# Kernel tuning notes

Hardware: AMD Instinct MI355X
Metric: run time of the kernel (lower is better)

Reference implementation:

```python
import jax, jax.numpy as jnp
import numpy as np

S, D, H = 2048, 1024, 16
DH = D // H
EPS = 1e-5


def setup_inputs() -> dict:
    key = jax.random.key(0)
    ks = jax.random.split(key, 6)
    scale = 0.02
    return {
        "inputs": jax.random.normal(ks[0], (S, D), dtype=jnp.float32),
        "ln_w": jnp.ones((D,), dtype=jnp.float32),
        "ln_b": jnp.zeros((D,), dtype=jnp.float32),
        "Wq": jax.random.normal(ks[1], (D, D), dtype=jnp.float32) * scale,
        "Wk": jax.random.normal(ks[2], (D, D), dtype=jnp.float32) * scale,
        "Wv": jax.random.normal(ks[3], (D, D), dtype=jnp.float32) * scale,
        "Wo": jax.random.normal(ks[4], (D, D), dtype=jnp.float32) * scale,
    }


def reference(inputs, ln_w, ln_b, Wq, Wk, Wv, Wo):
    # Pre-LayerNorm (per token), matching eqx.nn.LayerNorm (eps=1e-5)
    mu = jnp.mean(inputs, axis=-1, keepdims=True)
    var = jnp.var(inputs, axis=-1, keepdims=True)
    x = (inputs - mu) / jnp.sqrt(var + EPS) * ln_w + ln_b  # [S, D]

    # QKV projections (eqx Linear: y = W @ x, no bias) -> [S, H, DH]
    q = (x @ Wq.T).reshape(S, H, DH)
    k = (x @ Wk.T).reshape(S, H, DH)
    v = (x @ Wv.T).reshape(S, H, DH)

    # Scaled dot-product attention; softmax forced to full precision
    scores = jnp.einsum("shd,thd->hst", q, k) / jnp.sqrt(jnp.asarray(DH, x.dtype))
    attn = jax.nn.softmax(scores.astype(jnp.float32), axis=-1).astype(x.dtype)
    # (dropout is identity in inference mode)
    ctx = jnp.einsum("hst,thd->shd", attn, v).reshape(S, D)

    out = ctx @ Wo.T  # output projection
    # outer dropout is identity in inference mode; residual add
    return out + inputs
```

## Files before the change

### kernel.cpp

```cpp
#include <hip/hip_runtime.h>
#include <cstdint>
#include <cstddef>

typedef unsigned short u16;
typedef unsigned int u32;
typedef __attribute__((ext_vector_type(8))) short bf16x8;
typedef __attribute__((ext_vector_type(4))) short bf16x4;
typedef __attribute__((ext_vector_type(4))) float f32x4;
typedef __attribute__((ext_vector_type(4))) unsigned short u16x4;

#if __has_builtin(__builtin_amdgcn_mfma_f32_16x16x16bf16_1k)
#define MFMA16(a, b, c) __builtin_amdgcn_mfma_f32_16x16x16bf16_1k(a, b, c, 0, 0, 0)
#else
static __device__ __forceinline__ f32x4 mfma16_asm(bf16x4 a, bf16x4 b, f32x4 c) {
  asm volatile("v_mfma_f32_16x16x16_bf16 %0, %1, %2, %0\n\ts_nop 4"
               : "+v"(c) : "v"(a), "v"(b));
  return c;
}
#define MFMA16(a, b, c) mfma16_asm(a, b, c)
#endif

#if __has_builtin(__builtin_amdgcn_exp2f)
#define EXP2(x) __builtin_amdgcn_exp2f(x)
#else
#define EXP2(x) exp2f(x)
#endif

__device__ __forceinline__ u16 f2b(float f) {
  union { float f; unsigned u; } un; un.f = f;
  unsigned u = un.u;
  return (u16)((u + 0x7fffu + ((u >> 16) & 1u)) >> 16);
}

__device__ __forceinline__ u32 pkbf(float a, float b) {
  union { float f; u32 u; } ua, ub; ua.f = a; ub.f = b;
  return ((ua.u + 0x8000u) >> 16) | (((ub.u + 0x8000u) >> 16) << 16);
}

__device__ __forceinline__ void gload_lds16(const u16* g, u16* l) {
  __builtin_amdgcn_global_load_lds(
      (const __attribute__((address_space(1))) void*)g,
      (__attribute__((address_space(3))) void*)l, 16, 0, 0);
}

__device__ __forceinline__ void gemm128x64(
    const u16* __restrict__ A, const u16* __restrict__ B,
    u16* smA, u16* smB, int bm, int bn,
    float* outf, u16* outb, const float* __restrict__ resid, int ostride)
{
  const int tid = threadIdx.x;
  const int wave = tid >> 6, lane = tid & 63;
  const int quad = lane >> 4, l16 = lane & 15;
  const int wm = wave >> 1, wn = wave & 1;

  f32x4 acc[4][2];
  const f32x4 zero4 = {0.f, 0.f, 0.f, 0.f};
#pragma unroll
  for (int i = 0; i < 4; i++)
#pragma unroll
    for (int j = 0; j < 2; j++) acc[i][j] = zero4;

  const u16* Ab = A + (size_t)(bm * 128) * 1024;
  const u16* Bb = B + (size_t)(bn * 64) * 1024;

#define PSTAGE(buf, k0)                                                          \
  {                                                                              \
    _Pragma("unroll")                                                            \
    for (int ks = 0; ks < 2; ks++) {                                             \
      _Pragma("unroll")                                                          \
      for (int r = 0; r < 2; r++) {                                              \
        const int c = r * 256 + wave * 64 + lane;                                \
        gload_lds16(Ab + (size_t)(c >> 2) * 1024 + (k0) + ks * 32 + (c & 3) * 8, \
                    smA + (buf) * 8192 + ks * 4096 + (size_t)(r * 256 + wave * 64) * 8); \
      }                                                                          \
      const int c2 = wave * 64 + lane;                                           \
      gload_lds16(Bb + (size_t)(c2 >> 2) * 1024 + (k0) + ks * 32 + (c2 & 3) * 8, \
                  smB + (buf) * 4096 + ks * 2048 + (size_t)(wave * 64) * 8);     \
    }                                                                            \
  }

  PSTAGE(0, 0);
  __syncthreads();
  for (int t = 0; t < 16; t++) {
    const int cur = t & 1;
    if (t < 15) PSTAGE(cur ^ 1, (t + 1) * 64);
    const u16* sa = smA + cur * 8192;
    const u16* sb = smB + cur * 4096;
#pragma unroll
    for (int ks = 0; ks < 2; ks++) {
      bf16x8 afr[4], bfr[2];
#pragma unroll
      for (int tt = 0; tt < 4; tt++)
        afr[tt] = *(const bf16x8*)(sa + ks * 4096 + (wm * 64 + tt * 16 + l16) * 32 + quad * 8);
#pragma unroll
      for (int tt = 0; tt < 2; tt++)
        bfr[tt] = *(const bf16x8*)(sb + ks * 2048 + (wn * 32 + tt * 16 + l16) * 32 + quad * 8);
#pragma unroll
      for (int mt = 0; mt < 4; mt++)
#pragma unroll
        for (int nt = 0; nt < 2; nt++)
          acc[mt][nt] = __builtin_amdgcn_mfma_f32_16x16x32_bf16(afr[mt], bfr[nt], acc[mt][nt], 0, 0, 0);
    }
    __syncthreads();
  }
#undef PSTAGE

#pragma unroll
  for (int mt = 0; mt < 4; mt++)
#pragma unroll
    for (int nt = 0; nt < 2; nt++)
#pragma unroll
      for (int r = 0; r < 4; r++) {
        const int row = bm * 128 + wm * 64 + mt * 16 + quad * 4 + r;
        const int col = bn * 64 + wn * 32 + nt * 16 + l16;
        if (outb) outb[(size_t)row * ostride + col] = f2b(acc[mt][nt][r]);
        else outf[(size_t)row * ostride + col] =
                 acc[mt][nt][r] + resid[(size_t)row * ostride + col];
      }
}

__global__ __launch_bounds__(256, 3) void proj_k(
    const u16* __restrict__ xb, const u16* __restrict__ Wb,
    u16* __restrict__ qkbuf, u16* __restrict__ vTb)
{
  __shared__ u16 smA[2 * 128 * 64];
  __shared__ u16 smB[2 * 64 * 64];
  int b = blockIdx.x;
  const u16 *A, *B; u16* o; int bm, bn;
  if (b < 512) {
    const int c = b & 7, i = b >> 3;
    bm = ((c >> 2) << 3) | (i & 7);
    bn = ((c & 3) << 3) | (i >> 3);
    A = xb; B = Wb; o = qkbuf;
  } else {
    b -= 512;
    const int c = b & 7, i = b >> 3;
    bm = i & 7;
    bn = (c << 2) | (i >> 3);
    A = Wb + (size_t)2 * (1 << 20); B = xb; o = vTb;
  }
  gemm128x64(A, B, smA, smB, bm, bn, nullptr, o, nullptr, 2048);
}

__global__ __launch_bounds__(256, 3) void out_k(
    const u16* __restrict__ ctxb, const u16* __restrict__ Wob,
    float* __restrict__ out, const float* __restrict__ x)
{
  __shared__ u16 smA[2 * 128 * 64];
  __shared__ u16 smB[2 * 64 * 64];
  const int b = blockIdx.x;
  const int c = b & 7, i = b >> 3;
  const int bm = ((c >> 2) << 3) | (i & 7);
  const int bn = ((c & 3) << 2) | (i >> 3);
  gemm128x64(ctxb, Wob, smA, smB, bm, bn, out, nullptr, x, 1024);
}

__global__ __launch_bounds__(256) void pre_k(
    const float* __restrict__ x, const float* __restrict__ lnw, const float* __restrict__ lnb,
    const float* __restrict__ w0, const float* __restrict__ w1,
    const float* __restrict__ w2, const float* __restrict__ w3,
    u16* __restrict__ xb, u16* __restrict__ Wb)
{
  const int b = blockIdx.x;
  const int tid = threadIdx.x;
  if (b < 2048) {
    const int s = b;
    const float4 v = ((const float4*)(x + (size_t)s * 1024))[tid];
    float sum = v.x + v.y + v.z + v.w;
    float sq  = v.x * v.x + v.y * v.y + v.z * v.z + v.w * v.w;
#pragma unroll
    for (int off = 32; off >= 1; off >>= 1) {
      sum += __shfl_down(sum, off);
      sq  += __shfl_down(sq, off);
    }
    __shared__ float sS[4], sQ[4];
    const int wave = tid >> 6, lane = tid & 63;
    if (lane == 0) { sS[wave] = sum; sQ[wave] = sq; }
    __syncthreads();
    const float ts = sS[0] + sS[1] + sS[2] + sS[3];
    const float tq = sQ[0] + sQ[1] + sQ[2] + sQ[3];
    const float mu = ts * (1.0f / 1024.0f);
    const float var = tq * (1.0f / 1024.0f) - mu * mu;
    const float rstd = rsqrtf(var + 1e-5f);
    const float4 wv = ((const float4*)lnw)[tid];
    const float4 bv = ((const float4*)lnb)[tid];
    u16x4 o;
    o[0] = f2b((v.x - mu) * rstd * wv.x + bv.x);
    o[1] = f2b((v.y - mu) * rstd * wv.y + bv.y);
    o[2] = f2b((v.z - mu) * rstd * wv.z + bv.z);
    o[3] = f2b((v.w - mu) * rstd * wv.w + bv.w);
    *(u16x4*)(xb + (size_t)s * 1024 + tid * 4) = o;
  } else {
    const unsigned i = (unsigned)(b - 2048) * 1024u + tid * 4u;
    const unsigned NW = 1u << 20;
    const float* src; unsigned loc; float sc;
    if (i < NW)            { src = w0; loc = i;           sc = 0.18033688f; }
    else if (i < 2u * NW)  { src = w1; loc = i - NW;      sc = 1.0f; }
    else if (i < 3u * NW)  { src = w2; loc = i - 2u * NW; sc = 1.0f; }
    else                   { src = w3; loc = i - 3u * NW; sc = 1.0f; }
    const float4 v = *(const float4*)(src + loc);
    u16x4 r;
    r[0] = f2b(v.x * sc); r[1] = f2b(v.y * sc); r[2] = f2b(v.z * sc); r[3] = f2b(v.w * sc);
    *(u16x4*)(Wb + i) = r;
  }
}

__global__ __launch_bounds__(256, 2) void attn_k(
    const u16* __restrict__ qkbuf,
    const u16* __restrict__ vT,
    u16* __restrict__ ctx)
{
  const int bid = blockIdx.x;
  const int work = (bid & 7) * 64 + (bid >> 3);
  const int h = work >> 5;
  const int q0 = (work & 31) * 64;
  __shared__ __align__(16) unsigned char arena[65536];
  u16* kvbuf = (u16*)arena;
  const int tid = threadIdx.x;
  const int wave = tid >> 6, lane = tid & 63;
  const int quad = lane >> 4, l16 = lane & 15;
  const int a7 = l16 & 7;
  const u16* kg = qkbuf + 1024;

  bf16x8 qf[4][2];
#pragma unroll
  for (int s = 0; s < 4; s++)
#pragma unroll
    for (int ks = 0; ks < 2; ks++)
      qf[s][ks] = *(const bf16x8*)(qkbuf + (size_t)(q0 + s * 16 + l16) * 2048 + h * 64 + ks * 32 + quad * 8);

  const f32x4 zero4 = {0.f, 0.f, 0.f, 0.f};
  f32x4 Oacc[4][4];
#pragma unroll
  for (int s = 0; s < 4; s++)
#pragma unroll
    for (int dt = 0; dt < 4; dt++) Oacc[s][dt] = zero4;
  float lacc[4] = {0.f, 0.f, 0.f, 0.f};

#define STAGE(T, bf)                                                                     \
  {                                                                                      \
    _Pragma("unroll")                                                                    \
    for (int i = 0; i < 4; i++) {                                                        \
      const int idx = (wave * 4 + i) * 64 + lane;                                        \
      const int kt = idx >> 3, kc = (idx & 7) ^ (kt & 7);                                \
      gload_lds16(kg + (size_t)((T) * 128 + kt) * 2048 + h * 64 + kc * 8,                \
                  kvbuf + (bf) * 16384 + (size_t)(wave * 4 + i) * 512);                  \
      const int vd = idx >> 4, vc = (idx & 15) ^ (vd & 7);                               \
      gload_lds16(vT + (size_t)(h * 64 + vd) * 2048 + (T) * 128 + vc * 8,                \
                  kvbuf + (bf) * 16384 + 8192 + (size_t)(wave * 4 + i) * 512);           \
    }                                                                                    \
  }

  STAGE(0, 0);
  __syncthreads();

  for (int T = 0; T < 16; T++) {
    const int bf = T & 1;
    if (T + 1 < 16) STAGE(T + 1, 1 - bf);
    const u16* kb = kvbuf + bf * 16384;
    const u16* vb = kb + 8192;

    f32x4 st[2][4];
#pragma unroll
    for (int ntl = 0; ntl < 2; ntl++) {
      const int nt = wave * 2 + ntl;
      const u16* kr = kb + (nt * 16 + l16) * 64;
      const bf16x8 ka0 = *(const bf16x8*)(kr + (quad ^ a7) * 8);
      const bf16x8 ka1 = *(const bf16x8*)(kr + ((4 + quad) ^ a7) * 8);
#pragma unroll
      for (int s = 0; s < 4; s++) {
        f32x4 t0 = __builtin_amdgcn_mfma_f32_16x16x32_bf16(ka0, qf[s][0], zero4, 0, 0, 0);
        st[ntl][s] = __builtin_amdgcn_mfma_f32_16x16x32_bf16(ka1, qf[s][1], t0, 0, 0, 0);
      }
    }

    bf16x4 pk[2][4];
#pragma unroll
    for (int ntl = 0; ntl < 2; ntl++)
#pragma unroll
      for (int s = 0; s < 4; s++) {
        const float p0 = EXP2(st[ntl][s][0]);
        const float p1 = EXP2(st[ntl][s][1]);
        const float p2 = EXP2(st[ntl][s][2]);
        const float p3 = EXP2(st[ntl][s][3]);
        lacc[s] += (p0 + p1) + (p2 + p3);
        union { u32 u[2]; bf16x4 v; } pp;
        pp.u[0] = pkbf(p0, p1);
        pp.u[1] = pkbf(p2, p3);
        pk[ntl][s] = pp.v;
      }

#pragma unroll
    for (int ntl = 0; ntl < 2; ntl++)
#pragma unroll
      for (int dt = 0; dt < 4; dt++) {
        const bf16x4 bv = *(const bf16x4*)(vb + (dt * 16 + l16) * 128 +
            (((wave * 4 + ntl * 2 + (quad >> 1)) ^ a7) * 8 + (quad & 1) * 4));
#pragma unroll
        for (int s = 0; s < 4; s++)
          Oacc[s][dt] = MFMA16(pk[ntl][s], bv, Oacc[s][dt]);
      }
    __syncthreads();
  }
#undef STAGE

  float* rl = (float*)arena;
#pragma unroll
  for (int s = 0; s < 4; s++) {
    float l = lacc[s];
    l += __shfl_xor(l, 16);
    l += __shfl_xor(l, 32);
    if (quad == 0) rl[wave * 64 + s * 16 + l16] = l;
  }
  __syncthreads();
  const int m = tid >> 2, dg = (tid & 3) * 16;
  const float inv = 1.0f / (rl[m] + rl[64 + m] + rl[128 + m] + rl[192 + m]);
  __syncthreads();

  float* ro = (float*)arena;
#pragma unroll
  for (int s = 0; s < 4; s++)
#pragma unroll
    for (int dt = 0; dt < 4; dt++)
#pragma unroll
      for (int r = 0; r < 4; r++) {
        const int mr = s * 16 + quad * 4 + r;
        const int dc = (dt * 16 + l16) ^ ((mr & 7) << 1);
        ro[wave * 4096 + mr * 64 + dc] = Oacc[s][dt][r];
      }
  __syncthreads();
  u16* dst = ctx + (size_t)(q0 + m) * 1024 + h * 64 + dg;
  const int msw = (m & 7) << 1;
#pragma unroll
  for (int g = 0; g < 4; g++) {
    u16x4 o;
#pragma unroll
    for (int j = 0; j < 4; j++) {
      const int dc = (dg + g * 4 + j) ^ msw;
      const int base = m * 64 + dc;
      const float v = ro[base] + ro[4096 + base] + ro[8192 + base] + ro[12288 + base];
      o[j] = f2b(v * inv);
    }
    *(u16x4*)(dst + g * 4) = o;
  }
}

extern "C" void kernel_launch(void* const* d_in, const int* in_sizes, int n_in,
                              void* d_out, int out_size, void* d_ws, size_t ws_size,
                              hipStream_t stream)
{
  const float* x   = (const float*)d_in[0];
  const float* lnw = (const float*)d_in[1];
  const float* lnb = (const float*)d_in[2];
  const float* Wq  = (const float*)d_in[3];
  const float* Wk  = (const float*)d_in[4];
  const float* Wv  = (const float*)d_in[5];
  const float* Wo  = (const float*)d_in[6];

  u16* ws    = (u16*)d_ws;
  u16* xb    = ws;
  u16* Wb    = xb + (size_t)2048 * 1024;
  u16* qkbuf = Wb + (size_t)4 * 1024 * 1024;
  u16* vTb   = qkbuf + (size_t)2048 * 2048;
  u16* ctxb  = vTb + (size_t)1024 * 2048;

  pre_k<<<6144, 256, 0, stream>>>(x, lnw, lnb, Wq, Wk, Wv, Wo, xb, Wb);
  proj_k<<<768, 256, 0, stream>>>(xb, Wb, qkbuf, vTb);
  attn_k<<<512, 256, 0, stream>>>(qkbuf, vTb, ctxb);
  out_k<<<256, 256, 0, stream>>>(ctxb, Wb + (size_t)3 * (1 << 20), (float*)d_out, x);
}
```

Measured before the change: 153.8 us.

## Enlarge GEMM tiles to 128x128 with XOR-swizzled LDS layout

The projection and output GEMMs now use 128x128 block tiles instead of 128x64, so each wave computes 64x64 and each loaded fragment is reused more. The LDS staging layout changes from two 32-wide k-slabs to a 64-wide row with an XOR swizzle, which is meant to avoid bank conflicts on fragment reads. The grids are halved (384 and 128 blocks) and occupancy drops to two blocks per SM. On a GPU with this many CUs, 128 blocks for out_k may leave many CUs idle.

Measured after the change: 150.8 us. -2.0%, faster.

```diff
diff --git a/kernel.cpp b/kernel.cpp
--- a/kernel.cpp
+++ b/kernel.cpp
@@ -43,7 +43,7 @@
       (__attribute__((address_space(3))) void*)l, 16, 0, 0);
 }
 
-__device__ __forceinline__ void gemm128x64(
+__device__ __forceinline__ void gemm128x128(
     const u16* __restrict__ A, const u16* __restrict__ B,
     u16* smA, u16* smB, int bm, int bn,
     float* outf, u16* outb, const float* __restrict__ resid, int ostride)
@@ -53,29 +53,27 @@
   const int quad = lane >> 4, l16 = lane & 15;
   const int wm = wave >> 1, wn = wave & 1;
 
-  f32x4 acc[4][2];
+  f32x4 acc[4][4];
   const f32x4 zero4 = {0.f, 0.f, 0.f, 0.f};
 #pragma unroll
   for (int i = 0; i < 4; i++)
 #pragma unroll
-    for (int j = 0; j < 2; j++) acc[i][j] = zero4;
+    for (int j = 0; j < 4; j++) acc[i][j] = zero4;
 
   const u16* Ab = A + (size_t)(bm * 128) * 1024;
-  const u16* Bb = B + (size_t)(bn * 64) * 1024;
+  const u16* Bb = B + (size_t)(bn * 128) * 1024;
 
 #define PSTAGE(buf, k0)                                                          \
   {                                                                              \
     _Pragma("unroll")                                                            \
-    for (int ks = 0; ks < 2; ks++) {                                             \
-      _Pragma("unroll")                                                          \
-      for (int r = 0; r < 2; r++) {                                              \
-        const int c = r * 256 + wave * 64 + lane;                                \
-        gload_lds16(Ab + (size_t)(c >> 2) * 1024 + (k0) + ks * 32 + (c & 3) * 8, \
-                    smA + (buf) * 8192 + ks * 4096 + (size_t)(r * 256 + wave * 64) * 8); \
-      }                                                                          \
-      const int c2 = wave * 64 + lane;                                           \
-      gload_lds16(Bb + (size_t)(c2 >> 2) * 1024 + (k0) + ks * 32 + (c2 & 3) * 8, \
-                  smB + (buf) * 4096 + ks * 2048 + (size_t)(wave * 64) * 8);     \
+    for (int i = 0; i < 4; i++) {                                                \
+      const int idx = i * 256 + tid;                                             \
+      const int row = idx >> 3, sl = idx & 7;                                    \
+      const int g = (sl ^ (row & 7)) * 8;                                        \
+      gload_lds16(Ab + (size_t)row * 1024 + (k0) + g,                            \
+                  smA + (buf) * 8192 + (size_t)(i * 256 + wave * 64) * 8);       \
+      gload_lds16(Bb + (size_t)row * 1024 + (k0) + g,                            \
+                  smB + (buf) * 8192 + (size_t)(i * 256 + wave * 64) * 8);       \
     }                                                                            \
   }
 
@@ -85,20 +83,21 @@
     const int cur = t & 1;
     if (t < 15) PSTAGE(cur ^ 1, (t + 1) * 64);
     const u16* sa = smA + cur * 8192;
-    const u16* sb = smB + cur * 4096;
+    const u16* sb = smB + cur * 8192;
 #pragma unroll
     for (int ks = 0; ks < 2; ks++) {
-      bf16x8 afr[4], bfr[2];
-#pragma unroll
-      for (int tt = 0; tt < 4; tt++)
-        afr[tt] = *(const bf16x8*)(sa + ks * 4096 + (wm * 64 + tt * 16 + l16) * 32 + quad * 8);
-#pragma unroll
-      for (int tt = 0; tt < 2; tt++)
-        bfr[tt] = *(const bf16x8*)(sb + ks * 2048 + (wn * 32 + tt * 16 + l16) * 32 + quad * 8);
+      const int swz = ((ks * 4 + quad) ^ (l16 & 7)) * 8;
+      bf16x8 afr[4], bfr[4];
 #pragma unroll
       for (int mt = 0; mt < 4; mt++)
-#pragma unroll
-        for (int nt = 0; nt < 2; nt++)
+        afr[mt] = *(const bf16x8*)(sa + (wm * 64 + mt * 16 + l16) * 64 + swz);
+#pragma unroll
+      for (int nt = 0; nt < 4; nt++)
+        bfr[nt] = *(const bf16x8*)(sb + (wn * 64 + nt * 16 + l16) * 64 + swz);
+#pragma unroll
+      for (int mt = 0; mt < 4; mt++)
+#pragma unroll
+        for (int nt = 0; nt < 4; nt++)
           acc[mt][nt] = __builtin_amdgcn_mfma_f32_16x16x32_bf16(afr[mt], bfr[nt], acc[mt][nt], 0, 0, 0);
     }
     __syncthreads();
@@ -108,51 +107,51 @@
 #pragma unroll
   for (int mt = 0; mt < 4; mt++)
 #pragma unroll
-    for (int nt = 0; nt < 2; nt++)
+    for (int nt = 0; nt < 4; nt++)
 #pragma unroll
       for (int r = 0; r < 4; r++) {
         const int row = bm * 128 + wm * 64 + mt * 16 + quad * 4 + r;
-        const int col = bn * 64 + wn * 32 + nt * 16 + l16;
+        const int col = bn * 128 + wn * 64 + nt * 16 + l16;
         if (outb) outb[(size_t)row * ostride + col] = f2b(acc[mt][nt][r]);
         else outf[(size_t)row * ostride + col] =
                  acc[mt][nt][r] + resid[(size_t)row * ostride + col];
       }
 }
 
-__global__ __launch_bounds__(256, 3) void proj_k(
+__global__ __launch_bounds__(256, 2) void proj_k(
     const u16* __restrict__ xb, const u16* __restrict__ Wb,
     u16* __restrict__ qkbuf, u16* __restrict__ vTb)
 {
   __shared__ u16 smA[2 * 128 * 64];
-  __shared__ u16 smB[2 * 64 * 64];
+  __shared__ u16 smB[2 * 128 * 64];
   int b = blockIdx.x;
   const u16 *A, *B; u16* o; int bm, bn;
-  if (b < 512) {
+  if (b < 256) {
     const int c = b & 7, i = b >> 3;
     bm = ((c >> 2) << 3) | (i & 7);
-    bn = ((c & 3) << 3) | (i >> 3);
+    bn = ((c & 3) << 2) | (i >> 3);
     A = xb; B = Wb; o = qkbuf;
   } else {
-    b -= 512;
+    b -= 256;
     const int c = b & 7, i = b >> 3;
     bm = i & 7;
-    bn = (c << 2) | (i >> 3);
+    bn = (c << 1) | (i >> 3);
     A = Wb + (size_t)2 * (1 << 20); B = xb; o = vTb;
   }
-  gemm128x64(A, B, smA, smB, bm, bn, nullptr, o, nullptr, 2048);
-}
-
-__global__ __launch_bounds__(256, 3) void out_k(
+  gemm128x128(A, B, smA, smB, bm, bn, nullptr, o, nullptr, 2048);
+}
+
+__global__ __launch_bounds__(256, 2) void out_k(
     const u16* __restrict__ ctxb, const u16* __restrict__ Wob,
     float* __restrict__ out, const float* __restrict__ x)
 {
   __shared__ u16 smA[2 * 128 * 64];
-  __shared__ u16 smB[2 * 64 * 64];
+  __shared__ u16 smB[2 * 128 * 64];
   const int b = blockIdx.x;
   const int c = b & 7, i = b >> 3;
   const int bm = ((c >> 2) << 3) | (i & 7);
-  const int bn = ((c & 3) << 2) | (i >> 3);
-  gemm128x64(ctxb, Wob, smA, smB, bm, bn, out, nullptr, x, 1024);
+  const int bn = ((c & 3) << 1) | (i >> 3);
+  gemm128x128(ctxb, Wob, smA, smB, bm, bn, out, nullptr, x, 1024);
 }
 
 __global__ __launch_bounds__(256) void pre_k(
@@ -365,7 +364,7 @@
   u16* ctxb  = vTb + (size_t)1024 * 2048;
 
   pre_k<<<6144, 256, 0, stream>>>(x, lnw, lnb, Wq, Wk, Wv, Wo, xb, Wb);
-  proj_k<<<768, 256, 0, stream>>>(xb, Wb, qkbuf, vTb);
+  proj_k<<<384, 256, 0, stream>>>(xb, Wb, qkbuf, vTb);
   attn_k<<<512, 256, 0, stream>>>(qkbuf, vTb, ctxb);
-  out_k<<<256, 256, 0, stream>>>(ctxb, Wb + (size_t)3 * (1 << 20), (float*)d_out, x);
-}
+  out_k<<<128, 256, 0, stream>>>(ctxb, Wb + (size_t)3 * (1 << 20), (float*)d_out, x);
+}
```
